# Kernel tuning notes

Measured on AMD Instinct MI355X. Metric: run time of the kernel, lower is better.

Reference implementation:

```python
import jax, jax.numpy as jnp
import numpy as np

N = 50000      # num_nodes
DEG = 16       # edges per node
E = N * DEG    # 800k edges
IN_DIM = 512
OUT_DIM = 128


def _glorot(key, shape):
    limit = np.sqrt(6.0 / (shape[0] + shape[1]))
    return jax.random.uniform(key, shape, jnp.float32, -limit, limit)


def setup_inputs() -> dict:
    key = jax.random.key(0)
    k1, k2, k3 = jax.random.split(key, 3)
    x = jax.random.normal(k1, (N, IN_DIM), jnp.float32)
    W = _glorot(k2, (IN_DIM, OUT_DIM))
    a = _glorot(k3, (OUT_DIM, 1))
    # structured, duplicate-free edge list: node i -> (i+1..i+DEG) mod N
    rows = np.repeat(np.arange(N, dtype=np.int32), DEG)
    offs = np.tile(np.arange(1, DEG + 1, dtype=np.int32), N)
    cols = (rows + offs) % N
    edge_index = jnp.asarray(np.stack([rows, cols]), jnp.int32)  # [2, E]
    return {"x": x, "W": W, "a": a, "edge_index": edge_index}


def reference(x, W, a, edge_index):
    # sparse mm (math-identical dense form); dropout_rate=0 -> identity
    h = x @ W                                    # [N, OUT]
    rows, cols = edge_index[0], edge_index[1]
    h_i = h[rows]                                # [E, OUT] gather
    h_j = h[cols]                                # [E, OUT] gather
    scores = jax.nn.relu(jnp.abs(h_i - h_j) @ a)[:, 0]  # [E]
    # sparse row-wise softmax (segment softmax over destination rows)
    m = jax.ops.segment_max(scores, rows, num_segments=N)   # [N]
    p = jnp.exp(scores - m[rows])                            # [E]
    s = jax.ops.segment_sum(p, rows, num_segments=N)         # [N]
    attn = p / s[rows]                                       # [E]
    return h, attn
```

## Files before the change

### kernel.cpp

```cpp
#include <hip/hip_runtime.h>
#include <hip/hip_bf16.h>

#define NNODES 50000
#define DEG 16
#define NEDGES (NNODES * DEG)
#define IND 512
#define OUTD 128

#define BM 32
#define CK 64
#define NCH 8
#define NB 64
#define SROWS 80

typedef __attribute__((ext_vector_type(8))) short bf16x8;
typedef __attribute__((ext_vector_type(4))) float f32x4;

static __device__ __forceinline__ unsigned short f2bf(float f) {
    unsigned u = __builtin_bit_cast(unsigned, f);
    u += 0x7fffu + ((u >> 16) & 1u);
    return (unsigned short)(u >> 16);
}

static __device__ __forceinline__ bf16x8 pack8(float4 a, float4 b) {
    union { unsigned u[4]; bf16x8 v; } r;
    r.u[0] = (unsigned)f2bf(a.x) | ((unsigned)f2bf(a.y) << 16);
    r.u[1] = (unsigned)f2bf(a.z) | ((unsigned)f2bf(a.w) << 16);
    r.u[2] = (unsigned)f2bf(b.x) | ((unsigned)f2bf(b.y) << 16);
    r.u[3] = (unsigned)f2bf(b.z) | ((unsigned)f2bf(b.w) << 16);
    return r.v;
}

__global__ __launch_bounds__(256) void wt_kernel(const float* __restrict__ W,
                                                 unsigned short* __restrict__ Wt) {
    int flat = blockIdx.x * 256 + threadIdx.x;
    int n  = flat >> 7;
    int k4 = flat & 127;
    int k0 = k4 * 4;
    unsigned short v0 = f2bf(W[(k0 + 0) * OUTD + n]);
    unsigned short v1 = f2bf(W[(k0 + 1) * OUTD + n]);
    unsigned short v2 = f2bf(W[(k0 + 2) * OUTD + n]);
    unsigned short v3 = f2bf(W[(k0 + 3) * OUTD + n]);
    uint2 o;
    o.x = (unsigned)v0 | ((unsigned)v1 << 16);
    o.y = (unsigned)v2 | ((unsigned)v3 << 16);
    *reinterpret_cast<uint2*>(&Wt[n * IND + k0]) = o;
}

__global__ __launch_bounds__(256, 3) void gemm_kernel(const float* __restrict__ x,
                                                      const unsigned short* __restrict__ Wt,
                                                      float* __restrict__ h) {
    __shared__ __align__(16) unsigned char lds_[49152];

    const int tid  = threadIdx.x;
    const int lane = tid & 63;
    const int wid  = tid >> 6;
    const int l15  = lane & 15;
    const int kg   = lane >> 4;

    const int nwg = gridDim.x;
    const int q8  = nwg >> 3, r8 = nwg & 7;
    const int xcd = blockIdx.x & 7, idx = blockIdx.x >> 3;
    const int swz = (xcd < r8 ? xcd * (q8 + 1) : r8 * (q8 + 1) + (xcd - r8) * q8) + idx;
    const int base = swz * BM;

    const int rb = (wid >> 1) * 16;
    const int cb = (wid & 1) * 64;

    f32x4 acc[4];
#pragma unroll
    for (int nt = 0; nt < 4; ++nt) acc[nt] = (f32x4){0.f, 0.f, 0.f, 0.f};

    auto stage = [&](int buf, int ch) {
        for (int i = wid; i < 24; i += 4) {
            if (i < 8) {
                int row   = i * 4 + (lane >> 4);
                int lg    = (lane & 15) ^ (row & 7);
                int grow  = base + row; if (grow > NNODES - 1) grow = NNODES - 1;
                const float* gp = &x[(size_t)grow * IND + ch * CK + lg * 4];
                unsigned char* lp = &lds_[buf * 8192 + i * 1024];
                __builtin_amdgcn_global_load_lds((const unsigned int*)gp, (unsigned int*)lp, 16, 0, 0);
            } else {
                int i2  = i - 8;
                int col = i2 * 8 + (lane >> 3);
                int lg  = (lane & 7) ^ (col & 7);
                const unsigned short* gp = &Wt[(size_t)col * IND + ch * CK + lg * 8];
                unsigned char* lp = &lds_[16384 + buf * 16384 + i2 * 1024];
                __builtin_amdgcn_global_load_lds((const unsigned int*)gp, (unsigned int*)lp, 16, 0, 0);
            }
        }
    };

    stage(0, 0);
    __syncthreads();

    int buf = 0;
    for (int ch = 0; ch < NCH; ++ch) {
        if (ch < NCH - 1) stage(buf ^ 1, ch + 1);

#pragma unroll
        for (int ks = 0; ks < 2; ++ks) {
            int arow = rb + l15;
            int s1   = (ks * 8 + kg * 2) ^ (arow & 7);
            const unsigned char* ab = &lds_[buf * 8192 + arow * 256];
            float4 a1 = *reinterpret_cast<const float4*>(ab + s1 * 16);
            float4 a2 = *reinterpret_cast<const float4*>(ab + (s1 ^ 1) * 16);
            bf16x8 af = pack8(a1, a2);
#pragma unroll
            for (int nt = 0; nt < 4; ++nt) {
                int col = cb + nt * 16 + l15;
                int sB  = (ks * 4 + kg) ^ (col & 7);
                bf16x8 bv = *reinterpret_cast<const bf16x8*>(
                    &lds_[16384 + buf * 16384 + col * 128 + sB * 16]);
                acc[nt] = __builtin_amdgcn_mfma_f32_16x16x32_bf16(af, bv, acc[nt], 0, 0, 0);
            }
        }
        __syncthreads();
        buf ^= 1;
    }

#pragma unroll
    for (int nt = 0; nt < 4; ++nt) {
#pragma unroll
        for (int q = 0; q < 4; ++q) {
            int grow = base + rb + kg * 4 + q;
            if (grow < NNODES)
                h[(size_t)grow * OUTD + cb + nt * 16 + l15] = acc[nt][q];
        }
    }
}

__global__ __launch_bounds__(256) void edge_kernel(const float* __restrict__ h,
                                                   const float* __restrict__ a,
                                                   const int* __restrict__ eidx,
                                                   float* __restrict__ attn) {
    extern __shared__ __align__(16) unsigned char hl[];

    const int tid  = threadIdx.x;
    const int base = blockIdx.x * NB;
    const int lane = tid & 63;
    const int wid  = tid >> 6;
    const int j    = lane >> 2;
    const int g    = lane & 3;

    float4 a4[8];
#pragma unroll
    for (int c = 0; c < 8; ++c)
        a4[c] = *reinterpret_cast<const float4*>(&a[c * 16 + g * 4]);

    for (int p = 0; p < 10; ++p) {
        int f    = p * 256 + tid;
        int row  = f >> 5;
        int blkp = f & 31;
        int blk  = blkp ^ ((row & 7) << 2);
        int gr   = base + row;
        if (gr >= NNODES) gr -= NNODES;
        float4 v = *reinterpret_cast<const float4*>(&h[(size_t)gr * OUTD + blk * 4]);
        *reinterpret_cast<float4*>(&hl[f * 16]) = v;
    }
    __syncthreads();

    const int* cols = eidx + NEDGES;
    for (int n = 0; n < 16; ++n) {
        int i = base + wid * 16 + n;
        if (i >= NNODES) break;
        int e   = i * DEG + j;
        int col = cols[e];
        int cr  = col - base;
        if (cr < 0) cr += NNODES;
        int ri = i - base;
        float s = 0.f;
        if (cr < SROWS) {
#pragma unroll
            for (int c = 0; c < 8; ++c) {
                int blk = c * 4 + g;
                float4 hi = *reinterpret_cast<const float4*>(&hl[ri * 512 + ((blk ^ ((ri & 7) << 2)) * 16)]);
                float4 hj = *reinterpret_cast<const float4*>(&hl[cr * 512 + ((blk ^ ((cr & 7) << 2)) * 16)]);
                s = fmaf(fabsf(hi.x - hj.x), a4[c].x, s);
                s = fmaf(fabsf(hi.y - hj.y), a4[c].y, s);
                s = fmaf(fabsf(hi.z - hj.z), a4[c].z, s);
                s = fmaf(fabsf(hi.w - hj.w), a4[c].w, s);
            }
        } else {
#pragma unroll
            for (int c = 0; c < 8; ++c) {
                int blk = c * 4 + g;
                float4 hi = *reinterpret_cast<const float4*>(&hl[ri * 512 + ((blk ^ ((ri & 7) << 2)) * 16)]);
                float4 hj = *reinterpret_cast<const float4*>(&h[(size_t)col * OUTD + blk * 4]);
                s = fmaf(fabsf(hi.x - hj.x), a4[c].x, s);
                s = fmaf(fabsf(hi.y - hj.y), a4[c].y, s);
                s = fmaf(fabsf(hi.z - hj.z), a4[c].z, s);
                s = fmaf(fabsf(hi.w - hj.w), a4[c].w, s);
            }
        }
        s += __shfl_xor(s, 1);
        s += __shfl_xor(s, 2);
        s = fmaxf(s, 0.f);
        float m = s;
        m = fmaxf(m, __shfl_xor(m, 4));
        m = fmaxf(m, __shfl_xor(m, 8));
        m = fmaxf(m, __shfl_xor(m, 16));
        m = fmaxf(m, __shfl_xor(m, 32));
        float pv = __expf(s - m);
        float S = pv;
        S += __shfl_xor(S, 4);
        S += __shfl_xor(S, 8);
        S += __shfl_xor(S, 16);
        S += __shfl_xor(S, 32);
        if (g == 0) attn[e] = pv / S;
    }
}

extern "C" void kernel_launch(void* const* d_in, const int* in_sizes, int n_in,
                              void* d_out, int out_size, void* d_ws, size_t ws_size,
                              hipStream_t stream) {
    const float* x  = (const float*)d_in[0];
    const float* W  = (const float*)d_in[1];
    const float* a  = (const float*)d_in[2];
    const int* eidx = (const int*)d_in[3];
    float* h    = (float*)d_out;
    float* attn = h + (size_t)NNODES * OUTD;
    unsigned short* Wt = (unsigned short*)d_ws;

    hipLaunchKernelGGL(wt_kernel, dim3(64), dim3(256), 0, stream, W, Wt);
    hipLaunchKernelGGL(gemm_kernel, dim3((NNODES + BM - 1) / BM), dim3(256), 0, stream, x, Wt, h);
    hipLaunchKernelGGL(edge_kernel, dim3((NNODES + NB - 1) / NB), dim3(256), SROWS * 512, stream,
                       h, a, eidx, attn);
}
```

Before: 70.79 us.

## Drop LDS staging in GEMM; per-wave 16-row tiles load operands directly from global

The GEMM kernel no longer stages x and W tiles in shared memory with double buffering and barriers. Each wave now owns 16 rows and all 128 output columns, loading its A fragment and all B fragments directly from global memory (relying on L2/L1 for W reuse), with 8 accumulators per wave. This removes LDS traffic, barriers and swizzle arithmetic. In exchange it loses explicit load/compute overlap, reads W redundantly from cache in every wave, and drops the XCD-aware block remap.

```diff
diff --git a/kernel.cpp b/kernel.cpp
--- a/kernel.cpp
+++ b/kernel.cpp
@@ -7,9 +7,7 @@
 #define IND 512
 #define OUTD 128
 
-#define BM 32
-#define CK 64
-#define NCH 8
+#define NWTILES 3125
 #define NB 64
 #define SROWS 80
 
@@ -47,87 +45,48 @@
     *reinterpret_cast<uint2*>(&Wt[n * IND + k0]) = o;
 }
 
-__global__ __launch_bounds__(256, 3) void gemm_kernel(const float* __restrict__ x,
+__global__ __launch_bounds__(256, 4) void gemm_kernel(const float* __restrict__ x,
                                                       const unsigned short* __restrict__ Wt,
                                                       float* __restrict__ h) {
-    __shared__ __align__(16) unsigned char lds_[49152];
-
-    const int tid  = threadIdx.x;
-    const int lane = tid & 63;
-    const int wid  = tid >> 6;
+    const int lane = threadIdx.x & 63;
+    const int wid  = threadIdx.x >> 6;
+    const int wt_  = blockIdx.x * 4 + wid;
+    if (wt_ >= NWTILES) return;
+    const int row0 = wt_ * 16;
     const int l15  = lane & 15;
     const int kg   = lane >> 4;
 
-    const int nwg = gridDim.x;
-    const int q8  = nwg >> 3, r8 = nwg & 7;
-    const int xcd = blockIdx.x & 7, idx = blockIdx.x >> 3;
-    const int swz = (xcd < r8 ? xcd * (q8 + 1) : r8 * (q8 + 1) + (xcd - r8) * q8) + idx;
-    const int base = swz * BM;
+    const float* ap = &x[(size_t)(row0 + l15) * IND + kg * 8];
+    const unsigned short* bp = &Wt[(size_t)l15 * IND + kg * 8];
 
-    const int rb = (wid >> 1) * 16;
-    const int cb = (wid & 1) * 64;
+    f32x4 acc[8];
+#pragma unroll
+    for (int nt = 0; nt < 8; ++nt) acc[nt] = (f32x4){0.f, 0.f, 0.f, 0.f};
 
-    f32x4 acc[4];
-#pragma unroll
-    for (int nt = 0; nt < 4; ++nt) acc[nt] = (f32x4){0.f, 0.f, 0.f, 0.f};
-
-    auto stage = [&](int buf, int ch) {
-        for (int i = wid; i < 24; i += 4) {
-            if (i < 8) {
-                int row   = i * 4 + (lane >> 4);
-                int lg    = (lane & 15) ^ (row & 7);
-                int grow  = base + row; if (grow > NNODES - 1) grow = NNODES - 1;
-                const float* gp = &x[(size_t)grow * IND + ch * CK + lg * 4];
-                unsigned char* lp = &lds_[buf * 8192 + i * 1024];
-                __builtin_amdgcn_global_load_lds((const unsigned int*)gp, (unsigned int*)lp, 16, 0, 0);
-            } else {
-                int i2  = i - 8;
-                int col = i2 * 8 + (lane >> 3);
-                int lg  = (lane & 7) ^ (col & 7);
-                const unsigned short* gp = &Wt[(size_t)col * IND + ch * CK + lg * 8];
-                unsigned char* lp = &lds_[16384 + buf * 16384 + i2 * 1024];
-                __builtin_amdgcn_global_load_lds((const unsigned int*)gp, (unsigned int*)lp, 16, 0, 0);
-            }
-        }
-    };
-
-    stage(0, 0);
-    __syncthreads();
-
-    int buf = 0;
-    for (int ch = 0; ch < NCH; ++ch) {
-        if (ch < NCH - 1) stage(buf ^ 1, ch + 1);
-
+    for (int ch = 0; ch < 8; ++ch) {
+        const int k0 = ch * 64;
 #pragma unroll
         for (int ks = 0; ks < 2; ++ks) {
-            int arow = rb + l15;
-            int s1   = (ks * 8 + kg * 2) ^ (arow & 7);
-            const unsigned char* ab = &lds_[buf * 8192 + arow * 256];
-            float4 a1 = *reinterpret_cast<const float4*>(ab + s1 * 16);
-            float4 a2 = *reinterpret_cast<const float4*>(ab + (s1 ^ 1) * 16);
-            bf16x8 af = pack8(a1, a2);
+            const int kk = k0 + ks * 32;
+            bf16x8 bfr[8];
 #pragma unroll
-            for (int nt = 0; nt < 4; ++nt) {
-                int col = cb + nt * 16 + l15;
-                int sB  = (ks * 4 + kg) ^ (col & 7);
-                bf16x8 bv = *reinterpret_cast<const bf16x8*>(
-                    &lds_[16384 + buf * 16384 + col * 128 + sB * 16]);
-                acc[nt] = __builtin_amdgcn_mfma_f32_16x16x32_bf16(af, bv, acc[nt], 0, 0, 0);
-            }
+            for (int nt = 0; nt < 8; ++nt)
+                bfr[nt] = *reinterpret_cast<const bf16x8*>(bp + (size_t)nt * 16 * IND + kk);
+            float4 a0 = *reinterpret_cast<const float4*>(ap + kk);
+            float4 a1 = *reinterpret_cast<const float4*>(ap + kk + 4);
+            bf16x8 af = pack8(a0, a1);
+#pragma unroll
+            for (int nt = 0; nt < 8; ++nt)
+                acc[nt] = __builtin_amdgcn_mfma_f32_16x16x32_bf16(af, bfr[nt], acc[nt], 0, 0, 0);
         }
-        __syncthreads();
-        buf ^= 1;
     }
 
+    float* hp = &h[(size_t)(row0 + kg * 4) * OUTD + l15];
 #pragma unroll
-    for (int nt = 0; nt < 4; ++nt) {
+    for (int q = 0; q < 4; ++q)
 #pragma unroll
-        for (int q = 0; q < 4; ++q) {
-            int grow = base + rb + kg * 4 + q;
-            if (grow < NNODES)
-                h[(size_t)grow * OUTD + cb + nt * 16 + l15] = acc[nt][q];
-        }
-    }
+        for (int nt = 0; nt < 8; ++nt)
+            hp[(size_t)q * OUTD + nt * 16] = acc[nt][q];
 }
 
 __global__ __launch_bounds__(256) void edge_kernel(const float* __restrict__ h,
@@ -223,7 +182,7 @@
     unsigned short* Wt = (unsigned short*)d_ws;
 
     hipLaunchKernelGGL(wt_kernel, dim3(64), dim3(256), 0, stream, W, Wt);
-    hipLaunchKernelGGL(gemm_kernel, dim3((NNODES + BM - 1) / BM), dim3(256), 0, stream, x, Wt, h);
+    hipLaunchKernelGGL(gemm_kernel, dim3((NWTILES + 3) / 4), dim3(256), 0, stream, x, Wt, h);
     hipLaunchKernelGGL(edge_kernel, dim3((NNODES + NB - 1) / NB), dim3(256), SROWS * 512, stream,
                        h, a, eidx, attn);
 }
```

Result: slower. 110.2 us (+55.7%).
